# Kernel optimization log

Measured on AMD Instinct MI355X. Metric: run time of the kernel, lower is better.

The kernel has to match this reference:

```python
import jax, jax.numpy as jnp
import numpy as np

N_HITS = 49152
HIT_F = 256
INST_F = 32
N_IT_CONST = 1024
Q_MIN = 0.5   # ObjCondensationLoss default q_min
S_B = 1.0     # ObjCondensationLoss default background strength


def setup_inputs() -> dict:
    key = jax.random.key(0)
    ks = jax.random.split(key, 6)
    x = jax.random.normal(ks[0], (N_HITS, HIT_F), jnp.float32)
    W_beta = jax.random.normal(ks[1], (HIT_F, 1), jnp.float32) / np.sqrt(HIT_F).astype(np.float32)
    b_beta = jnp.zeros((1,), jnp.float32)
    W_coord = jax.random.normal(ks[2], (HIT_F, INST_F), jnp.float32) / np.sqrt(HIT_F).astype(np.float32)
    b_coord = jnp.zeros((INST_F,), jnp.float32)
    temp = jnp.zeros((), jnp.float32)  # nn.Parameter(torch.tensor(0.0))
    # true instance labels per hit; pin first N_IT hits so every instance is populated
    y_i = jax.random.randint(ks[3], (N_HITS,), 0, N_IT_CONST)
    y_i = y_i.at[:N_IT_CONST].set(jnp.arange(N_IT_CONST))
    idx = jnp.arange(N_HITS)
    noise = (idx % 5 == 0) & (idx >= N_IT_CONST)
    y_i = jnp.where(noise, -1, y_i).astype(jnp.int64)
    y_semantic = jax.random.randint(ks[4], (N_HITS,), 0, 7).astype(jnp.int32)
    # hit -> true-instance membership edges (E_H_IT), fixed shape built eagerly
    yv = np.asarray(y_i)
    e0 = np.nonzero(yv >= 0)[0]
    edge_index = jnp.asarray(np.stack([e0, yv[e0]]), dtype=jnp.int32)
    return {"x": x, "W_beta": W_beta, "b_beta": b_beta, "W_coord": W_coord,
            "b_coord": b_coord, "temp": temp, "y_i": y_i,
            "y_semantic": y_semantic, "edge_index": edge_index, "n_it": N_IT_CONST}


def _obj_condensation_loss(ox, beta, y_i, edge_index, n_it):
    """Object condensation loss -> stack([background_loss, potential_loss])."""
    n = ox.shape[0]
    beta_c = jnp.clip(beta, 1e-4, 1.0 - 1e-4)
    q = jnp.arctanh(beta_c) ** 2 + Q_MIN  # charge per hit, [N]
    e_h, e_i = edge_index[0], edge_index[1]
    qe = q[e_h]
    # condensation point alpha_k = member hit with max charge (segment argmax)
    seg_max = jax.ops.segment_max(qe, e_i, num_segments=n_it)
    is_max = qe >= seg_max[e_i]
    alpha = jax.ops.segment_min(jnp.where(is_max, e_h, n), e_i, num_segments=n_it)
    alpha = jnp.clip(alpha, 0, n - 1)
    x_a = ox[alpha]        # [K, D]
    q_a = q[alpha]         # [K]
    beta_a = beta_c[alpha]  # [K]
    # attractive potential over membership edges: q_i * q_alpha * ||x_i - x_alpha||^2
    d2_att = jnp.sum((ox[e_h] - x_a[e_i]) ** 2, axis=-1)
    v_att = jnp.sum(qe * q_a[e_i] * d2_att)
    # repulsive potential over all (hit, instance) non-member pairs: hinge(1 - dist)
    d2 = (jnp.sum(ox * ox, axis=1)[:, None] + jnp.sum(x_a * x_a, axis=1)[None, :]
          - 2.0 * ox @ x_a.T)  # [N, K]
    dist = jnp.sqrt(jnp.maximum(d2, 0.0) + 1e-12)
    hinge = jnp.maximum(1.0 - dist, 0.0)
    member = jnp.zeros((n, n_it), jnp.float32).at[e_h, e_i].set(1.0)
    v_rep = jnp.sum((q[:, None] * q_a[None, :]) * hinge * (1.0 - member))
    l_v = (v_att + v_rep) / n
    # background loss: push beta_alpha -> 1, noise-hit beta -> 0
    noise = y_i < 0
    n_noise = jnp.maximum(jnp.sum(noise), 1)
    l_b = jnp.mean(1.0 - beta_a) + S_B * jnp.sum(jnp.where(noise, beta_c, 0.0)) / n_noise
    return jnp.stack([l_b, l_v])


def reference(x, W_beta, b_beta, W_coord, b_coord, temp, y_i, y_semantic, edge_index, n_it):
    beta = jax.nn.sigmoid(x @ W_beta + b_beta)[:, 0]  # h.of, [N]
    ox = x @ W_coord + b_coord                        # h.ox, [N, D]
    loss_vec = _obj_condensation_loss(ox, beta, y_i, edge_index, n_it)
    loss_vec = loss_vec * jnp.exp(-temp)  # temperature-weighted (b, v)
    return loss_vec.sum() + temp          # train-stage scalar loss
```

## Files before the change

### kernel.cpp

```cpp
#include <hip/hip_runtime.h>
#include <math.h>

#define NH 49152
#define KI 1024
#define DD 32
#define HF 256

#define WS_PART  0
#define WS_SEG64 8
#define WS_A12   (WS_SEG64 + 2*KI)
#define WS_H12   (WS_A12 + 12*KI)
#define WS_XA    (WS_H12 + 12*NH)
#define WS_OX    (WS_XA + KI*DD)

__global__ void k_init(float* __restrict__ ws) {
    int i = blockIdx.x * blockDim.x + threadIdx.x;
    if (i < KI) ((unsigned long long*)(ws + WS_SEG64))[i] = 0ull;
    if (i < 8) ws[WS_PART + i] = 0.0f;
}

template<bool G3>
__device__ __forceinline__ void chunk_compute(const float (*xs)[128], int l, int kbase, int g,
        const float* __restrict__ Wc, const float* __restrict__ Wb,
        float* acc, float& wA, float& wB) {
    #pragma unroll 8
    for (int kk = 0; kk < 32; ++kk) {
        const int K = ((kk >> 2) & 7) << 2;
        const float2 xv = *(const float2*)(&xs[kk][(2 * l) ^ K]);
        const int krow = kbase + kk;
        const float4 w0 = *(const float4*)(Wc + krow * 32 + g * 8);
        const float4 w1 = *(const float4*)(Wc + krow * 32 + g * 8 + 4);
        acc[0] = fmaf(xv.x, w0.x, acc[0]);   acc[8]  = fmaf(xv.y, w0.x, acc[8]);
        acc[1] = fmaf(xv.x, w0.y, acc[1]);   acc[9]  = fmaf(xv.y, w0.y, acc[9]);
        acc[2] = fmaf(xv.x, w0.z, acc[2]);   acc[10] = fmaf(xv.y, w0.z, acc[10]);
        acc[3] = fmaf(xv.x, w0.w, acc[3]);   acc[11] = fmaf(xv.y, w0.w, acc[11]);
        acc[4] = fmaf(xv.x, w1.x, acc[4]);   acc[12] = fmaf(xv.y, w1.x, acc[12]);
        acc[5] = fmaf(xv.x, w1.y, acc[5]);   acc[13] = fmaf(xv.y, w1.y, acc[13]);
        acc[6] = fmaf(xv.x, w1.z, acc[6]);   acc[14] = fmaf(xv.y, w1.z, acc[14]);
        acc[7] = fmaf(xv.x, w1.w, acc[7]);   acc[15] = fmaf(xv.y, w1.w, acc[15]);
        if (G3) { const float wb = Wb[krow]; wA = fmaf(xv.x, wb, wA); wB = fmaf(xv.y, wb, wB); }
    }
}

__global__ __launch_bounds__(256, 2) void k_gemm(
        const float* __restrict__ x, const float* __restrict__ Wb,
        const float* __restrict__ bb, const float* __restrict__ Wc,
        const float* __restrict__ bcrd, const int* __restrict__ yi,
        float* __restrict__ ws) {
    __shared__ float xsT[2][32][128];
    const int t  = threadIdx.x;
    const int g  = __builtin_amdgcn_readfirstlane(t >> 6);
    const int l  = t & 63;
    const int h0 = blockIdx.x * 128;

    const int sh = t >> 3;
    const int sq = t & 7;
    const int c0 = sh ^ (sq << 2);
    float4 r0, r1, r2, r3;
#define GLOAD(kc) { \
    const float* xp = x + (size_t)(h0 + sh) * HF + (kc) * 32 + sq * 4; \
    r0 = *(const float4*)(xp); \
    r1 = *(const float4*)(xp + 32 * HF); \
    r2 = *(const float4*)(xp + 64 * HF); \
    r3 = *(const float4*)(xp + 96 * HF); }
#define SSTORE(buf) { \
    float* bp = &xsT[buf][sq * 4][0]; \
    bp[c0]          = r0.x; bp[128 + c0]        = r0.y; bp[256 + c0]        = r0.z; bp[384 + c0]        = r0.w; \
    bp[c0 + 32]     = r1.x; bp[128 + c0 + 32]   = r1.y; bp[256 + c0 + 32]   = r1.z; bp[384 + c0 + 32]   = r1.w; \
    bp[c0 + 64]     = r2.x; bp[128 + c0 + 64]   = r2.y; bp[256 + c0 + 64]   = r2.z; bp[384 + c0 + 64]   = r2.w; \
    bp[c0 + 96]     = r3.x; bp[128 + c0 + 96]   = r3.y; bp[256 + c0 + 96]   = r3.z; bp[384 + c0 + 96]   = r3.w; }

    float acc[16];
    #pragma unroll
    for (int i = 0; i < 16; ++i) acc[i] = 0.0f;
    float wA = 0.0f, wB = 0.0f;

    GLOAD(0);
    SSTORE(0);
    __syncthreads();
    for (int kc = 0; kc < 8; ++kc) {
        if (kc < 7) GLOAD(kc + 1);
        if (g == 3) chunk_compute<true>(xsT[kc & 1], l, kc * 32, g, Wc, Wb, acc, wA, wB);
        else        chunk_compute<false>(xsT[kc & 1], l, kc * 32, g, Wc, Wb, acc, wA, wB);
        __syncthreads();
        if (kc < 7) { SSTORE((kc + 1) & 1); __syncthreads(); }
    }

    const int ha = h0 + 2 * l;
    const float4 bc0 = *(const float4*)(bcrd + g * 8);
    const float4 bc1 = *(const float4*)(bcrd + g * 8 + 4);
    float4 A0 = {acc[0] + bc0.x, acc[1] + bc0.y, acc[2] + bc0.z, acc[3] + bc0.w};
    float4 A1 = {acc[4] + bc1.x, acc[5] + bc1.y, acc[6] + bc1.z, acc[7] + bc1.w};
    float4 B0 = {acc[8] + bc0.x, acc[9] + bc0.y, acc[10] + bc0.z, acc[11] + bc0.w};
    float4 B1 = {acc[12] + bc1.x, acc[13] + bc1.y, acc[14] + bc1.z, acc[15] + bc1.w};
    *(float4*)(ws + WS_OX + (size_t)ha * DD + g * 8)           = A0;
    *(float4*)(ws + WS_OX + (size_t)ha * DD + g * 8 + 4)       = A1;
    *(float4*)(ws + WS_OX + (size_t)(ha + 1) * DD + g * 8)     = B0;
    *(float4*)(ws + WS_OX + (size_t)(ha + 1) * DD + g * 8 + 4) = B1;

    if (g == 0) {
        float sA = A0.x*A0.x + A0.y*A0.y + A0.z*A0.z + A0.w*A0.w
                 + A1.x*A1.x + A1.y*A1.y + A1.z*A1.z + A1.w*A1.w;
        float sB = B0.x*B0.x + B0.y*B0.y + B0.z*B0.z + B0.w*B0.w
                 + B1.x*B1.x + B1.y*B1.y + B1.z*B1.z + B1.w*B1.w;
        *(float4*)(ws + WS_H12 + (size_t)ha * 12)           = A0;
        *(float4*)(ws + WS_H12 + (size_t)ha * 12 + 4)       = A1;
        ws[WS_H12 + (size_t)ha * 12 + 8] = 0.5f * sA;
        *(float4*)(ws + WS_H12 + (size_t)(ha + 1) * 12)     = B0;
        *(float4*)(ws + WS_H12 + (size_t)(ha + 1) * 12 + 4) = B1;
        ws[WS_H12 + (size_t)(ha + 1) * 12 + 8] = 0.5f * sB;
    }
    if (g == 3) {
        const float bb0 = bb[0];
        float zA = wA + bb0, zB = wB + bb0;
        float bA = 1.0f / (1.0f + expf(-zA));
        float bB = 1.0f / (1.0f + expf(-zB));
        float bcA = fminf(fmaxf(bA, 1e-4f), 0.9999f);
        float bcB = fminf(fmaxf(bB, 1e-4f), 0.9999f);
        float atA = atanhf(bcA), atB = atanhf(bcB);
        ws[WS_H12 + (size_t)ha * 12 + 9]        = atA * atA + 0.5f;
        ws[WS_H12 + (size_t)ha * 12 + 10]       = bcA;
        ws[WS_H12 + (size_t)(ha + 1) * 12 + 9]  = atB * atB + 0.5f;
        ws[WS_H12 + (size_t)(ha + 1) * 12 + 10] = bcB;
        int yA = yi[ha], yB = yi[ha + 1];
        float    nb  = ((yA < 0) ? bcA : 0.0f) + ((yB < 0) ? bcB : 0.0f);
        unsigned cnt = (unsigned)(yA < 0) + (unsigned)(yB < 0);
        for (int off = 32; off > 0; off >>= 1) {
            nb  += __shfl_down(nb, off);
            cnt += __shfl_down(cnt, off);
        }
        if (l == 0) {
            atomicAdd(ws + WS_PART + 2, nb);
            atomicAdd((unsigned int*)(ws + WS_PART + 3), cnt);
        }
    }
}

__global__ __launch_bounds__(256) void k_segmax(const int* __restrict__ eh, const int* __restrict__ ei,
                                                int E, const float* __restrict__ h12,
                                                unsigned long long* __restrict__ seg) {
    int e = blockIdx.x * 256 + threadIdx.x;
    if (e < E) {
        int h = eh[e];
        float q = h12[(size_t)h * 12 + 9];
        unsigned long long pk = ((unsigned long long)__float_as_uint(q) << 32)
                              | (unsigned)(NH - 1 - h);
        atomicMax(seg + ei[e], pk);
    }
}

__global__ __launch_bounds__(256) void k_gather(float* __restrict__ ws) {
    const int k = blockIdx.x * 256 + threadIdx.x;
    unsigned long long pk = ((const unsigned long long*)(ws + WS_SEG64))[k];
    int a = NH - 1 - (int)(unsigned)(pk & 0xffffffffu);
    a = max(0, min(a, NH - 1));
    float4 v0, v1;
    float s8 = 0.0f;
    #pragma unroll
    for (int d0 = 0; d0 < DD; d0 += 4) {
        float4 v = *(const float4*)(ws + WS_OX + (size_t)a * DD + d0);
        *(float4*)(ws + WS_XA + (size_t)k * DD + d0) = v;
        if (d0 == 0) { v0 = v; s8 += v.x*v.x + v.y*v.y + v.z*v.z + v.w*v.w; }
        if (d0 == 4) { v1 = v; s8 += v.x*v.x + v.y*v.y + v.z*v.z + v.w*v.w; }
    }
    *(float4*)(ws + WS_A12 + (size_t)k * 12)     = v0;
    *(float4*)(ws + WS_A12 + (size_t)k * 12 + 4) = v1;
    ws[WS_A12 + (size_t)k * 12 + 8] = 0.5f * (s8 - 1.0f);
    ws[WS_A12 + (size_t)k * 12 + 9] = ws[WS_H12 + (size_t)a * 12 + 9];
    float omba = 1.0f - ws[WS_H12 + (size_t)a * 12 + 10];
    for (int off = 32; off > 0; off >>= 1) omba += __shfl_down(omba, off);
    if ((threadIdx.x & 63) == 0) atomicAdd(ws + WS_PART + 4, omba);
}

__global__ __launch_bounds__(256) void k_att(const int* __restrict__ eh, const int* __restrict__ ei,
                                             int E, float* __restrict__ ws) {
    const int t = threadIdx.x;
    const int e = blockIdx.x * 256 + t;
    float c = 0.0f;
    if (e < E) {
        const int h = eh[e], k = ei[e];
        const float* a = ws + WS_OX + (size_t)h * DD;
        const float* b = ws + WS_XA + (size_t)k * DD;
        float d2 = 0.0f;
        #pragma unroll
        for (int d0 = 0; d0 < DD; d0 += 4) {
            float4 av = *(const float4*)(a + d0);
            float4 bv = *(const float4*)(b + d0);
            float dx = av.x - bv.x; d2 = fmaf(dx, dx, d2);
            float dy = av.y - bv.y; d2 = fmaf(dy, dy, d2);
            float dz = av.z - bv.z; d2 = fmaf(dz, dz, d2);
            float dw = av.w - bv.w; d2 = fmaf(dw, dw, d2);
        }
        c = ws[WS_H12 + (size_t)h * 12 + 9] * ws[WS_A12 + (size_t)k * 12 + 9] * d2;
    }
    for (int off = 32; off > 0; off >>= 1) c += __shfl_down(c, off);
    __shared__ float red[4];
    if ((t & 63) == 0) red[t >> 6] = c;
    __syncthreads();
    if (t == 0) atomicAdd(ws + WS_PART + 1, red[0] + red[1] + red[2] + red[3]);
}

__global__ __launch_bounds__(256, 3) void k_rep(const int* __restrict__ yi,
        const float* __restrict__ a12, const float* __restrict__ h12,
        const float* __restrict__ ox, const float* __restrict__ xa,
        float* __restrict__ part) {
    const int t  = threadIdx.x;
    const int bh = blockIdx.x % 96;
    const int bk = blockIdx.x / 96;
    const int k0 = bk * 128;

    const int h1 = bh * 512 + t;
    const int h2 = h1 + 256;
    const float4 p0  = *(const float4*)(h12 + (size_t)h1 * 12);
    const float4 p1  = *(const float4*)(h12 + (size_t)h1 * 12 + 4);
    const float2 cq1 = *(const float2*)(h12 + (size_t)h1 * 12 + 8);
    const float4 s0  = *(const float4*)(h12 + (size_t)h2 * 12);
    const float4 s1  = *(const float4*)(h12 + (size_t)h2 * 12 + 4);
    const float2 cq2 = *(const float2*)(h12 + (size_t)h2 * 12 + 8);
    const int yh1 = yi[h1], yh2 = yi[h2];
    float loc = 0.0f;

    #pragma unroll 4
    for (int r = 0; r < 128; ++r) {
        const float* ap = a12 + (size_t)(k0 + r) * 12;
        const float4 b0  = *(const float4*)(ap);
        const float4 b1  = *(const float4*)(ap + 4);
        const float2 bcq = *(const float2*)(ap + 8);
        float acc1 = -cq1.x - bcq.x;
        acc1 = fmaf(p0.x, b0.x, acc1);
        acc1 = fmaf(p0.y, b0.y, acc1);
        acc1 = fmaf(p0.z, b0.z, acc1);
        acc1 = fmaf(p0.w, b0.w, acc1);
        acc1 = fmaf(p1.x, b1.x, acc1);
        acc1 = fmaf(p1.y, b1.y, acc1);
        acc1 = fmaf(p1.z, b1.z, acc1);
        acc1 = fmaf(p1.w, b1.w, acc1);
        float acc2 = -cq2.x - bcq.x;
        acc2 = fmaf(s0.x, b0.x, acc2);
        acc2 = fmaf(s0.y, b0.y, acc2);
        acc2 = fmaf(s0.z, b0.z, acc2);
        acc2 = fmaf(s0.w, b0.w, acc2);
        acc2 = fmaf(s1.x, b1.x, acc2);
        acc2 = fmaf(s1.y, b1.y, acc2);
        acc2 = fmaf(s1.z, b1.z, acc2);
        acc2 = fmaf(s1.w, b1.w, acc2);
        if (acc1 > 0.0f) {
            const int kg = k0 + r;
            if (yh1 != kg) {
                float d2 = 1.0f - 2.0f * acc1;
                const float* hp = ox + (size_t)h1 * DD;
                const float* apf = xa + (size_t)kg * DD;
                #pragma unroll
                for (int d = 8; d < DD; d += 4) {
                    float4 av = *(const float4*)(hp + d);
                    float4 bv = *(const float4*)(apf + d);
                    float dx = av.x - bv.x; d2 = fmaf(dx, dx, d2);
                    float dy = av.y - bv.y; d2 = fmaf(dy, dy, d2);
                    float dz = av.z - bv.z; d2 = fmaf(dz, dz, d2);
                    float dw = av.w - bv.w; d2 = fmaf(dw, dw, d2);
                }
                float dist = sqrtf(fmaxf(d2, 0.0f) + 1e-12f);
                float hin  = 1.0f - dist;
                if (hin > 0.0f) loc += cq1.y * bcq.y * hin;
            }
        }
        if (acc2 > 0.0f) {
            const int kg = k0 + r;
            if (yh2 != kg) {
                float d2 = 1.0f - 2.0f * acc2;
                const float* hp = ox + (size_t)h2 * DD;
                const float* apf = xa + (size_t)kg * DD;
                #pragma unroll
                for (int d = 8; d < DD; d += 4) {
                    float4 av = *(const float4*)(hp + d);
                    float4 bv = *(const float4*)(apf + d);
                    float dx = av.x - bv.x; d2 = fmaf(dx, dx, d2);
                    float dy = av.y - bv.y; d2 = fmaf(dy, dy, d2);
                    float dz = av.z - bv.z; d2 = fmaf(dz, dz, d2);
                    float dw = av.w - bv.w; d2 = fmaf(dw, dw, d2);
                }
                float dist = sqrtf(fmaxf(d2, 0.0f) + 1e-12f);
                float hin  = 1.0f - dist;
                if (hin > 0.0f) loc += cq2.y * bcq.y * hin;
            }
        }
    }
    for (int off = 32; off > 0; off >>= 1) loc += __shfl_down(loc, off);
    __shared__ float red[4];
    if ((t & 63) == 0) red[t >> 6] = loc;
    __syncthreads();
    if (t == 0) atomicAdd(part + 0, red[0] + red[1] + red[2] + red[3]);
}

__global__ void k_final(const float* __restrict__ temp, float* __restrict__ ws,
                        float* __restrict__ out) {
    float vrep  = ws[WS_PART + 0];
    float vatt  = ws[WS_PART + 1];
    float nsum  = ws[WS_PART + 2];
    unsigned nn = *(const unsigned int*)(ws + WS_PART + 3);
    float somba = ws[WS_PART + 4];
    float lb = somba * (1.0f / (float)KI) + nsum / (float)(nn < 1u ? 1u : nn);
    float lv = (vatt + vrep) / (float)NH;
    float tv = temp[0];
    out[0] = (lb + lv) * expf(-tv) + tv;
}

extern "C" void kernel_launch(void* const* d_in, const int* in_sizes, int n_in,
                              void* d_out, int out_size, void* d_ws, size_t ws_size,
                              hipStream_t stream) {
    const float* x    = (const float*)d_in[0];
    const float* Wb   = (const float*)d_in[1];
    const float* bb   = (const float*)d_in[2];
    const float* Wc   = (const float*)d_in[3];
    const float* bcrd = (const float*)d_in[4];
    const float* temp = (const float*)d_in[5];
    const int*   yi   = (const int*)d_in[6];
    const int*   ep   = (const int*)d_in[8];
    const int E = in_sizes[8] / 2;
    const int* eh = ep;
    const int* ei = ep + E;
    float* ws  = (float*)d_ws;
    float* out = (float*)d_out;

    k_init<<<4, 256, 0, stream>>>(ws);
    k_gemm<<<NH / 128, 256, 0, stream>>>(x, Wb, bb, Wc, bcrd, yi, ws);
    const int eb = (E + 255) / 256;
    k_segmax<<<eb, 256, 0, stream>>>(eh, ei, E, ws + WS_H12,
                                     (unsigned long long*)(ws + WS_SEG64));
    k_gather<<<KI / 256, 256, 0, stream>>>(ws);
    k_att<<<eb, 256, 0, stream>>>(eh, ei, E, ws);
    k_rep<<<96 * 8, 256, 0, stream>>>(yi, ws + WS_A12, ws + WS_H12,
                                      ws + WS_OX, ws + WS_XA, ws);
    k_final<<<1, 1, 0, stream>>>(temp, ws, out);
}
```

Measured before the change: 97.27 us.

## Split GEMM K dimension across two blocks with atomics and separate epilogue kernel

```diff
diff --git a/kernel.cpp b/kernel.cpp
--- a/kernel.cpp
+++ b/kernel.cpp
@@ -12,63 +12,47 @@
 #define WS_H12   (WS_A12 + 12*KI)
 #define WS_XA    (WS_H12 + 12*NH)
 #define WS_OX    (WS_XA + KI*DD)
-
-__global__ void k_init(float* __restrict__ ws) {
-    int i = blockIdx.x * blockDim.x + threadIdx.x;
-    if (i < KI) ((unsigned long long*)(ws + WS_SEG64))[i] = 0ull;
-    if (i < 8) ws[WS_PART + i] = 0.0f;
-}
-
-template<bool G3>
-__device__ __forceinline__ void chunk_compute(const float (*xs)[128], int l, int kbase, int g,
-        const float* __restrict__ Wc, const float* __restrict__ Wb,
-        float* acc, float& wA, float& wB) {
-    #pragma unroll 8
-    for (int kk = 0; kk < 32; ++kk) {
-        const int K = ((kk >> 2) & 7) << 2;
-        const float2 xv = *(const float2*)(&xs[kk][(2 * l) ^ K]);
-        const int krow = kbase + kk;
-        const float4 w0 = *(const float4*)(Wc + krow * 32 + g * 8);
-        const float4 w1 = *(const float4*)(Wc + krow * 32 + g * 8 + 4);
-        acc[0] = fmaf(xv.x, w0.x, acc[0]);   acc[8]  = fmaf(xv.y, w0.x, acc[8]);
-        acc[1] = fmaf(xv.x, w0.y, acc[1]);   acc[9]  = fmaf(xv.y, w0.y, acc[9]);
-        acc[2] = fmaf(xv.x, w0.z, acc[2]);   acc[10] = fmaf(xv.y, w0.z, acc[10]);
-        acc[3] = fmaf(xv.x, w0.w, acc[3]);   acc[11] = fmaf(xv.y, w0.w, acc[11]);
-        acc[4] = fmaf(xv.x, w1.x, acc[4]);   acc[12] = fmaf(xv.y, w1.x, acc[12]);
-        acc[5] = fmaf(xv.x, w1.y, acc[5]);   acc[13] = fmaf(xv.y, w1.y, acc[13]);
-        acc[6] = fmaf(xv.x, w1.z, acc[6]);   acc[14] = fmaf(xv.y, w1.z, acc[14]);
-        acc[7] = fmaf(xv.x, w1.w, acc[7]);   acc[15] = fmaf(xv.y, w1.w, acc[15]);
-        if (G3) { const float wb = Wb[krow]; wA = fmaf(xv.x, wb, wA); wB = fmaf(xv.y, wb, wB); }
-    }
-}
-
-__global__ __launch_bounds__(256, 2) void k_gemm(
+#define WS_ZB    (WS_OX + NH*DD)
+
+__global__ __launch_bounds__(256) void k_init(float* __restrict__ ws) {
+    const int i = blockIdx.x * 256 + threadIdx.x;
+    const float4 z4 = {0.0f, 0.0f, 0.0f, 0.0f};
+    *(float4*)(ws + WS_OX + (size_t)i * 4) = z4;
+    if (i < 12288) *(float4*)(ws + WS_ZB + (size_t)i * 4) = z4;
+    if (i < 512)   *(float4*)(ws + WS_SEG64 + (size_t)i * 4) = z4;
+    if (i == 0) { *(float4*)(ws + WS_PART) = z4; *(float4*)(ws + WS_PART + 4) = z4; }
+}
+
+__global__ __launch_bounds__(256, 3) void k_gemm(
         const float* __restrict__ x, const float* __restrict__ Wb,
         const float* __restrict__ bb, const float* __restrict__ Wc,
-        const float* __restrict__ bcrd, const int* __restrict__ yi,
-        float* __restrict__ ws) {
-    __shared__ float xsT[2][32][128];
+        const float* __restrict__ bcrd, float* __restrict__ ws) {
+    __shared__ float xsT[32][132];
     const int t  = threadIdx.x;
+    const int l  = t & 63;
     const int g  = __builtin_amdgcn_readfirstlane(t >> 6);
-    const int l  = t & 63;
-    const int h0 = blockIdx.x * 128;
-
-    const int sh = t >> 3;
-    const int sq = t & 7;
-    const int c0 = sh ^ (sq << 2);
-    float4 r0, r1, r2, r3;
-#define GLOAD(kc) { \
-    const float* xp = x + (size_t)(h0 + sh) * HF + (kc) * 32 + sq * 4; \
-    r0 = *(const float4*)(xp); \
-    r1 = *(const float4*)(xp + 32 * HF); \
-    r2 = *(const float4*)(xp + 64 * HF); \
-    r3 = *(const float4*)(xp + 96 * HF); }
-#define SSTORE(buf) { \
-    float* bp = &xsT[buf][sq * 4][0]; \
-    bp[c0]          = r0.x; bp[128 + c0]        = r0.y; bp[256 + c0]        = r0.z; bp[384 + c0]        = r0.w; \
-    bp[c0 + 32]     = r1.x; bp[128 + c0 + 32]   = r1.y; bp[256 + c0 + 32]   = r1.z; bp[384 + c0 + 32]   = r1.w; \
-    bp[c0 + 64]     = r2.x; bp[128 + c0 + 64]   = r2.y; bp[256 + c0 + 64]   = r2.z; bp[384 + c0 + 64]   = r2.w; \
-    bp[c0 + 96]     = r3.x; bp[128 + c0 + 96]   = r3.y; bp[256 + c0 + 96]   = r3.z; bp[384 + c0 + 96]   = r3.w; }
+    const int h0 = (blockIdx.x >> 1) * 128;
+    const int kh = blockIdx.x & 1;
+    const int K0 = kh * 128;
+
+    const int srow = t >> 3;
+    const int scol = (t & 7) * 4;
+    float4 rv0, rv1, rv2, rv3;
+#define GLOAD(c) { \
+    const float* xp = x + (size_t)(h0 + srow) * HF + K0 + (c) * 32 + scol; \
+    rv0 = *(const float4*)(xp); \
+    rv1 = *(const float4*)(xp + 32 * HF); \
+    rv2 = *(const float4*)(xp + 64 * HF); \
+    rv3 = *(const float4*)(xp + 96 * HF); }
+#define SSTORE() { \
+    xsT[scol+0][srow]    = rv0.x; xsT[scol+1][srow]    = rv0.y; \
+    xsT[scol+2][srow]    = rv0.z; xsT[scol+3][srow]    = rv0.w; \
+    xsT[scol+0][srow+32] = rv1.x; xsT[scol+1][srow+32] = rv1.y; \
+    xsT[scol+2][srow+32] = rv1.z; xsT[scol+3][srow+32] = rv1.w; \
+    xsT[scol+0][srow+64] = rv2.x; xsT[scol+1][srow+64] = rv2.y; \
+    xsT[scol+2][srow+64] = rv2.z; xsT[scol+3][srow+64] = rv2.w; \
+    xsT[scol+0][srow+96] = rv3.x; xsT[scol+1][srow+96] = rv3.y; \
+    xsT[scol+2][srow+96] = rv3.z; xsT[scol+3][srow+96] = rv3.w; }
 
     float acc[16];
     #pragma unroll
@@ -76,63 +60,85 @@
     float wA = 0.0f, wB = 0.0f;
 
     GLOAD(0);
-    SSTORE(0);
+    SSTORE();
     __syncthreads();
-    for (int kc = 0; kc < 8; ++kc) {
-        if (kc < 7) GLOAD(kc + 1);
-        if (g == 3) chunk_compute<true>(xsT[kc & 1], l, kc * 32, g, Wc, Wb, acc, wA, wB);
-        else        chunk_compute<false>(xsT[kc & 1], l, kc * 32, g, Wc, Wb, acc, wA, wB);
+    for (int c = 0; c < 4; ++c) {
+        if (c < 3) GLOAD(c + 1);
+        const int kb = K0 + c * 32;
+        #pragma unroll
+        for (int s = 0; s < 4; ++s) {
+            float2 xv[8];
+            #pragma unroll
+            for (int j = 0; j < 8; ++j)
+                xv[j] = *(const float2*)(&xsT[s * 8 + j][2 * l]);
+            const float* wp = Wc + (size_t)(kb + s * 8) * 32 + g * 8;
+            #pragma unroll
+            for (int j = 0; j < 8; ++j) {
+                const float w0 = wp[j * 32 + 0], w1 = wp[j * 32 + 1];
+                const float w2 = wp[j * 32 + 2], w3 = wp[j * 32 + 3];
+                const float w4 = wp[j * 32 + 4], w5 = wp[j * 32 + 5];
+                const float w6 = wp[j * 32 + 6], w7 = wp[j * 32 + 7];
+                acc[0] = fmaf(xv[j].x, w0, acc[0]);  acc[8]  = fmaf(xv[j].y, w0, acc[8]);
+                acc[1] = fmaf(xv[j].x, w1, acc[1]);  acc[9]  = fmaf(xv[j].y, w1, acc[9]);
+                acc[2] = fmaf(xv[j].x, w2, acc[2]);  acc[10] = fmaf(xv[j].y, w2, acc[10]);
+                acc[3] = fmaf(xv[j].x, w3, acc[3]);  acc[11] = fmaf(xv[j].y, w3, acc[11]);
+                acc[4] = fmaf(xv[j].x, w4, acc[4]);  acc[12] = fmaf(xv[j].y, w4, acc[12]);
+                acc[5] = fmaf(xv[j].x, w5, acc[5]);  acc[13] = fmaf(xv[j].y, w5, acc[13]);
+                acc[6] = fmaf(xv[j].x, w6, acc[6]);  acc[14] = fmaf(xv[j].y, w6, acc[14]);
+                acc[7] = fmaf(xv[j].x, w7, acc[7]);  acc[15] = fmaf(xv[j].y, w7, acc[15]);
+                if (g == 3) {
+                    const float wb = Wb[kb + s * 8 + j];
+                    wA = fmaf(xv[j].x, wb, wA);
+                    wB = fmaf(xv[j].y, wb, wB);
+                }
+            }
+        }
         __syncthreads();
-        if (kc < 7) { SSTORE((kc + 1) & 1); __syncthreads(); }
+        if (c < 3) { SSTORE(); __syncthreads(); }
     }
 
     const int ha = h0 + 2 * l;
-    const float4 bc0 = *(const float4*)(bcrd + g * 8);
-    const float4 bc1 = *(const float4*)(bcrd + g * 8 + 4);
-    float4 A0 = {acc[0] + bc0.x, acc[1] + bc0.y, acc[2] + bc0.z, acc[3] + bc0.w};
-    float4 A1 = {acc[4] + bc1.x, acc[5] + bc1.y, acc[6] + bc1.z, acc[7] + bc1.w};
-    float4 B0 = {acc[8] + bc0.x, acc[9] + bc0.y, acc[10] + bc0.z, acc[11] + bc0.w};
-    float4 B1 = {acc[12] + bc1.x, acc[13] + bc1.y, acc[14] + bc1.z, acc[15] + bc1.w};
-    *(float4*)(ws + WS_OX + (size_t)ha * DD + g * 8)           = A0;
-    *(float4*)(ws + WS_OX + (size_t)ha * DD + g * 8 + 4)       = A1;
-    *(float4*)(ws + WS_OX + (size_t)(ha + 1) * DD + g * 8)     = B0;
-    *(float4*)(ws + WS_OX + (size_t)(ha + 1) * DD + g * 8 + 4) = B1;
-
-    if (g == 0) {
-        float sA = A0.x*A0.x + A0.y*A0.y + A0.z*A0.z + A0.w*A0.w
-                 + A1.x*A1.x + A1.y*A1.y + A1.z*A1.z + A1.w*A1.w;
-        float sB = B0.x*B0.x + B0.y*B0.y + B0.z*B0.z + B0.w*B0.w
-                 + B1.x*B1.x + B1.y*B1.y + B1.z*B1.z + B1.w*B1.w;
-        *(float4*)(ws + WS_H12 + (size_t)ha * 12)           = A0;
-        *(float4*)(ws + WS_H12 + (size_t)ha * 12 + 4)       = A1;
-        ws[WS_H12 + (size_t)ha * 12 + 8] = 0.5f * sA;
-        *(float4*)(ws + WS_H12 + (size_t)(ha + 1) * 12)     = B0;
-        *(float4*)(ws + WS_H12 + (size_t)(ha + 1) * 12 + 4) = B1;
-        ws[WS_H12 + (size_t)(ha + 1) * 12 + 8] = 0.5f * sB;
+    #pragma unroll
+    for (int c = 0; c < 8; ++c) {
+        const float b = (kh == 0) ? bcrd[g * 8 + c] : 0.0f;
+        atomicAdd(ws + WS_OX + (size_t)ha * DD + g * 8 + c,       acc[c] + b);
+        atomicAdd(ws + WS_OX + (size_t)(ha + 1) * DD + g * 8 + c, acc[8 + c] + b);
     }
     if (g == 3) {
-        const float bb0 = bb[0];
-        float zA = wA + bb0, zB = wB + bb0;
-        float bA = 1.0f / (1.0f + expf(-zA));
-        float bB = 1.0f / (1.0f + expf(-zB));
-        float bcA = fminf(fmaxf(bA, 1e-4f), 0.9999f);
-        float bcB = fminf(fmaxf(bB, 1e-4f), 0.9999f);
-        float atA = atanhf(bcA), atB = atanhf(bcB);
-        ws[WS_H12 + (size_t)ha * 12 + 9]        = atA * atA + 0.5f;
-        ws[WS_H12 + (size_t)ha * 12 + 10]       = bcA;
-        ws[WS_H12 + (size_t)(ha + 1) * 12 + 9]  = atB * atB + 0.5f;
-        ws[WS_H12 + (size_t)(ha + 1) * 12 + 10] = bcB;
-        int yA = yi[ha], yB = yi[ha + 1];
-        float    nb  = ((yA < 0) ? bcA : 0.0f) + ((yB < 0) ? bcB : 0.0f);
-        unsigned cnt = (unsigned)(yA < 0) + (unsigned)(yB < 0);
-        for (int off = 32; off > 0; off >>= 1) {
-            nb  += __shfl_down(nb, off);
-            cnt += __shfl_down(cnt, off);
-        }
-        if (l == 0) {
-            atomicAdd(ws + WS_PART + 2, nb);
-            atomicAdd((unsigned int*)(ws + WS_PART + 3), cnt);
-        }
+        const float zb = (kh == 0) ? bb[0] : 0.0f;
+        atomicAdd(ws + WS_ZB + ha,     wA + zb);
+        atomicAdd(ws + WS_ZB + ha + 1, wB + zb);
+    }
+}
+
+__global__ __launch_bounds__(256) void k_epi(const int* __restrict__ yi,
+                                             float* __restrict__ ws) {
+    const int h = blockIdx.x * 256 + threadIdx.x;
+    const float* oxr = ws + WS_OX + (size_t)h * DD;
+    const float4 o0 = *(const float4*)(oxr);
+    const float4 o1 = *(const float4*)(oxr + 4);
+    const float s8 = o0.x*o0.x + o0.y*o0.y + o0.z*o0.z + o0.w*o0.w
+                   + o1.x*o1.x + o1.y*o1.y + o1.z*o1.z + o1.w*o1.w;
+    float* hr = ws + WS_H12 + (size_t)h * 12;
+    *(float4*)(hr)     = o0;
+    *(float4*)(hr + 4) = o1;
+    hr[8] = 0.5f * s8;
+    const float z    = ws[WS_ZB + h];
+    const float beta = 1.0f / (1.0f + expf(-z));
+    const float bcv  = fminf(fmaxf(beta, 1e-4f), 0.9999f);
+    const float at   = atanhf(bcv);
+    hr[9]  = at * at + 0.5f;
+    hr[10] = bcv;
+    const int y = yi[h];
+    float    nb  = (y < 0) ? bcv : 0.0f;
+    unsigned cnt = (y < 0) ? 1u : 0u;
+    for (int off = 32; off > 0; off >>= 1) {
+        nb  += __shfl_down(nb, off);
+        cnt += __shfl_down(cnt, off);
+    }
+    if ((threadIdx.x & 63) == 0) {
+        atomicAdd(ws + WS_PART + 2, nb);
+        atomicAdd((unsigned int*)(ws + WS_PART + 3), cnt);
     }
 }
 
@@ -200,14 +206,19 @@
     if (t == 0) atomicAdd(ws + WS_PART + 1, red[0] + red[1] + red[2] + red[3]);
 }
 
-__global__ __launch_bounds__(256, 3) void k_rep(const int* __restrict__ yi,
+__global__ __launch_bounds__(256, 4) void k_rep(const int* __restrict__ yi,
         const float* __restrict__ a12, const float* __restrict__ h12,
         const float* __restrict__ ox, const float* __restrict__ xa,
         float* __restrict__ part) {
+    __shared__ float al[128 * 12];
     const int t  = threadIdx.x;
     const int bh = blockIdx.x % 96;
     const int bk = blockIdx.x / 96;
     const int k0 = bk * 128;
+
+    for (int i = t; i < 128 * 12; i += 256)
+        al[i] = a12[(size_t)k0 * 12 + i];
+    __syncthreads();
 
     const int h1 = bh * 512 + t;
     const int h2 = h1 + 256;
@@ -222,10 +233,9 @@
 
     #pragma unroll 4
     for (int r = 0; r < 128; ++r) {
-        const float* ap = a12 + (size_t)(k0 + r) * 12;
-        const float4 b0  = *(const float4*)(ap);
-        const float4 b1  = *(const float4*)(ap + 4);
-        const float2 bcq = *(const float2*)(ap + 8);
+        const float4 b0  = *(const float4*)(al + r * 12);
+        const float4 b1  = *(const float4*)(al + r * 12 + 4);
+        const float2 bcq = *(const float2*)(al + r * 12 + 8);
         float acc1 = -cq1.x - bcq.x;
         acc1 = fmaf(p0.x, b0.x, acc1);
         acc1 = fmaf(p0.y, b0.y, acc1);
@@ -248,7 +258,7 @@
             const int kg = k0 + r;
             if (yh1 != kg) {
                 float d2 = 1.0f - 2.0f * acc1;
-                const float* hp = ox + (size_t)h1 * DD;
+                const float* hp  = ox + (size_t)h1 * DD;
                 const float* apf = xa + (size_t)kg * DD;
                 #pragma unroll
                 for (int d = 8; d < DD; d += 4) {
@@ -268,7 +278,7 @@
             const int kg = k0 + r;
             if (yh2 != kg) {
                 float d2 = 1.0f - 2.0f * acc2;
-                const float* hp = ox + (size_t)h2 * DD;
+                const float* hp  = ox + (size_t)h2 * DD;
                 const float* apf = xa + (size_t)kg * DD;
                 #pragma unroll
                 for (int d = 8; d < DD; d += 4) {
@@ -322,8 +332,9 @@
     float* ws  = (float*)d_ws;
     float* out = (float*)d_out;
 
-    k_init<<<4, 256, 0, stream>>>(ws);
-    k_gemm<<<NH / 128, 256, 0, stream>>>(x, Wb, bb, Wc, bcrd, yi, ws);
+    k_init<<<1536, 256, 0, stream>>>(ws);
+    k_gemm<<<(NH / 128) * 2, 256, 0, stream>>>(x, Wb, bb, Wc, bcrd, ws);
+    k_epi<<<NH / 256, 256, 0, stream>>>(yi, ws);
     const int eb = (E + 255) / 256;
     k_segmax<<<eb, 256, 0, stream>>>(eh, ei, E, ws + WS_H12,
                                      (unsigned long long*)(ws + WS_SEG64));
```

Result: slower. 260.9 us (+168.2%).
